# Performance work log

Hardware: AMD Instinct MI355X
Metric: run time of the kernel (lower is better)

## Reference

```python
import jax, jax.numpy as jnp
import numpy as np


def setup_inputs() -> dict:
    key = jax.random.key(0)
    k1, k2, k3 = jax.random.split(key, 3)
    B, M, K, C = 4, 64, 32, 256
    ch, red = K * K, 2
    x = jax.random.normal(k1, (B, M, K, C), dtype=jnp.float32)
    # 1x1 conv weights (bias=False): squeeze spatial dims -> plain matrices
    W1 = jax.random.normal(k2, (ch // red, ch), dtype=jnp.float32) * 0.02
    W2 = jax.random.normal(k3, (ch, ch // red), dtype=jnp.float32) * 0.02
    return {"x": x, "W1": W1, "W2": W2}


def reference(x, W1, W2):
    B, M, K, C = x.shape
    # ---- Pearson correlation (Bessel-corrected), matches self.pearson ----
    cen = x - x.mean(axis=-1, keepdims=True)                       # [B,M,K,C]
    cov = jnp.einsum('bmic,bmjc->bmij', cen, cen) / (C - 1)         # [B,M,K,K]
    std = jnp.sqrt(jnp.sum(cen * cen, axis=-1) / (C - 1))           # [B,M,K]
    adj = cov / (std[..., :, None] * std[..., None, :])             # [B,M,K,K]
    # ---- attention scores: concat([x_i, pos*x_j]) then avgpool over 2C ----
    # pos = 1 where x_i == x_j elementwise else 2
    xi = x[:, :, :, None, :]                                        # [B,M,K,1,C]
    xj = x[:, :, None, :, :]                                        # [B,M,1,K,C]
    pos = jnp.where(xi == xj, jnp.float32(1.0), jnp.float32(2.0))   # [B,M,K,K,C]
    # AdaptiveAvgPool2d((None,1)) over the 2C concat = mean of both halves
    pooled = 0.5 * (x.mean(-1)[:, :, :, None] + jnp.mean(pos * xj, axis=-1))  # [B,M,K,K]
    # conv input channel index is i*K+j -> reshape to [B, K*K, M]
    p = pooled.transpose(0, 2, 3, 1).reshape(B, K * K, M)
    h = jax.nn.gelu(jnp.einsum('oc,bcm->bom', W1, p), approximate=False)
    e = jax.nn.sigmoid(jnp.einsum('oc,bcm->bom', W2, h))            # [B,K*K,M]
    e = e.transpose(0, 2, 1).reshape(B, M, K, K)
    # ---- masked softmax + aggregation ----
    NEG = jnp.float32(-9e15)
    attention = jax.nn.softmax(jnp.where(adj > 0, e, NEG), axis=-1)
    out = jnp.einsum('bmij,bmjc->bmic', attention, x)               # [B,M,K,C]
    return out, adj
```

## Files before the change

kernel.cpp:

```cpp
#include <hip/hip_runtime.h>
#include <math.h>

#define KK 32
#define CC 256

__global__ __launch_bounds__(256) void prep_kernel(
    const float* __restrict__ x, float* __restrict__ mean_ws,
    float* __restrict__ adj_out)
{
    __shared__ float xs[KK][258];
    __shared__ float part8[256];
    __shared__ float meanv[KK];
    __shared__ float covm[KK][KK + 1];
    __shared__ float stdv[KK];

    const int t  = threadIdx.x;
    const int bm = blockIdx.x;
    const int b  = bm >> 6, m = bm & 63;
    const float* xp = x + (size_t)bm * (KK * CC);

    #pragma unroll
    for (int s = 0; s < 8; ++s) {
        const int e = s * 1024 + t * 4;
        const float4 v = *(const float4*)(xp + e);
        const int i = e >> 8, col = e & 255;
        xs[i][col] = v.x; xs[i][col + 1] = v.y;
        xs[i][col + 2] = v.z; xs[i][col + 3] = v.w;
    }
    __syncthreads();
    {
        const int i = t >> 3, part = t & 7;
        float s = 0.f;
        const int c0 = part * 32;
        #pragma unroll
        for (int c = 0; c < 32; ++c) s += xs[i][c0 + c];
        part8[t] = s;
    }
    __syncthreads();
    if (t < KK) {
        float s = 0.f;
        #pragma unroll
        for (int k = 0; k < 8; ++k) s += part8[t * 8 + k];
        meanv[t] = s * (1.0f / CC);
        mean_ws[(size_t)(b * 32 + t) * 64 + m] = meanv[t];
    }
    __syncthreads();
    {
        const int r = t >> 3, c0 = (t & 7) * 32;
        const float mv = meanv[r];
        #pragma unroll
        for (int c = 0; c < 32; ++c) xs[r][c0 + c] -= mv;
    }
    __syncthreads();
    if (t < 136) {
        int rem = t, r = 0;
        while (rem >= 16 - r) { rem -= 16 - r; ++r; }
        const int ti = r, tj = r + rem;
        const int i0 = 2 * ti, i1 = i0 + 1, j0 = 2 * tj, j1 = j0 + 1;
        float c00 = 0.f, c01 = 0.f, c10 = 0.f, c11 = 0.f;
        for (int c = 0; c < CC; c += 2) {
            const float2 a0 = *(const float2*)&xs[i0][c];
            const float2 a1 = *(const float2*)&xs[i1][c];
            const float2 b0 = *(const float2*)&xs[j0][c];
            const float2 b1 = *(const float2*)&xs[j1][c];
            c00 += a0.x * b0.x; c00 += a0.y * b0.y;
            c01 += a0.x * b1.x; c01 += a0.y * b1.y;
            c10 += a1.x * b0.x; c10 += a1.y * b0.y;
            c11 += a1.x * b1.x; c11 += a1.y * b1.y;
        }
        c00 *= (1.0f / (CC - 1)); c01 *= (1.0f / (CC - 1));
        c10 *= (1.0f / (CC - 1)); c11 *= (1.0f / (CC - 1));
        covm[i0][j0] = c00; covm[i0][j1] = c01;
        covm[i1][j0] = c10; covm[i1][j1] = c11;
        covm[j0][i0] = c00; covm[j1][i0] = c01;
        covm[j0][i1] = c10; covm[j1][i1] = c11;
    }
    __syncthreads();
    if (t < KK) stdv[t] = sqrtf(covm[t][t]);
    __syncthreads();
    #pragma unroll
    for (int k = 0; k < 4; ++k) {
        const int pair = t + k * 256;
        const int i = pair >> 5, j = pair & 31;
        adj_out[(size_t)bm * 1024 + pair] = covm[i][j] / (stdv[i] * stdv[j]);
    }
}

__global__ __launch_bounds__(64) void mlp1_kernel(
    const float* __restrict__ W1, const float* __restrict__ mean_ws,
    float* __restrict__ h_ws)
{
    __shared__ float rowlds[4][1056];
    __shared__ float Al[4][32];
    const int t  = threadIdx.x;
    const int b  = blockIdx.y;
    const int ob = blockIdx.x * 4;

    const float* wr = W1 + (size_t)ob * 1024;
    #pragma unroll
    for (int u = 0; u < 16; ++u) {
        const int e4 = t + u * 64;
        const int q  = e4 >> 8;
        const int e  = (e4 & 255) * 4;
        const float4 v = *(const float4*)(wr + q * 1024 + e);
        const int f = (e >> 5) * 33 + (e & 31);
        rowlds[q][f] = v.x; rowlds[q][f + 1] = v.y;
        rowlds[q][f + 2] = v.z; rowlds[q][f + 3] = v.w;
    }
    __syncthreads();
    {
        const int k = t & 31, qh = t >> 5;
        #pragma unroll
        for (int qq = 0; qq < 2; ++qq) {
            const int q = qh + qq * 2;
            float rs = 0.f, cs = 0.f;
            #pragma unroll
            for (int j = 0; j < 32; ++j) rs += rowlds[q][k * 33 + j];
            #pragma unroll
            for (int i = 0; i < 32; ++i) cs += rowlds[q][i * 33 + k];
            Al[q][k] = 0.5f * rs + cs - 0.5f * rowlds[q][k * 34];
        }
    }
    __syncthreads();
    const int m = t;
    float mr[32];
    #pragma unroll
    for (int k = 0; k < 32; ++k) mr[k] = mean_ws[(size_t)(b * 32 + k) * 64 + m];
    #pragma unroll
    for (int q = 0; q < 4; ++q) {
        float a = 0.f;
        #pragma unroll
        for (int k = 0; k < 32; ++k) a += Al[q][k] * mr[k];
        const float g = 0.5f * a * (1.0f + erff(a * 0.70710678118654752f));
        h_ws[(size_t)(b * 512 + ob + q) * 64 + m] = g;
    }
}

__global__ __launch_bounds__(256) void mlp2_kernel(
    const float* __restrict__ W2, const float* __restrict__ h_ws,
    float* __restrict__ e_ws)
{
    __shared__ float W2s[16][512];
    const int m  = threadIdx.x;
    const int ow = threadIdx.y;
    const int b  = blockIdx.y;
    const int ob = blockIdx.x * 16;

    {
        const int t = ow * 64 + m;
        const float* src = W2 + (size_t)ob * 512;
        #pragma unroll
        for (int u = 0; u < 8; ++u) {
            const int e4 = t + u * 256;
            const float4 v = *(const float4*)(src + e4 * 4);
            *(float4*)&W2s[e4 >> 7][(e4 & 127) * 4] = v;
        }
    }
    __syncthreads();

    const float* hb = h_ws + (size_t)b * 512 * 64 + m;
    float acc[4] = {0.f, 0.f, 0.f, 0.f};
    const int ol = ow * 4;

    for (int c = 0; c < 512; c += 4) {
        const float hv0 = hb[(size_t)(c + 0) * 64];
        const float hv1 = hb[(size_t)(c + 1) * 64];
        const float hv2 = hb[(size_t)(c + 2) * 64];
        const float hv3 = hb[(size_t)(c + 3) * 64];
        #pragma unroll
        for (int q = 0; q < 4; ++q) {
            const float4 w = *(const float4*)&W2s[ol + q][c];
            acc[q] += w.x * hv0;
            acc[q] += w.y * hv1;
            acc[q] += w.z * hv2;
            acc[q] += w.w * hv3;
        }
    }
    float4 sv;
    sv.x = 1.0f / (1.0f + expf(-acc[0]));
    sv.y = 1.0f / (1.0f + expf(-acc[1]));
    sv.z = 1.0f / (1.0f + expf(-acc[2]));
    sv.w = 1.0f / (1.0f + expf(-acc[3]));
    *(float4*)&e_ws[(size_t)(b * 64 + m) * 1024 + ob + ol] = sv;
}

__global__ __launch_bounds__(256) void softmax_out_kernel(
    const float* __restrict__ x, const float* __restrict__ e_ws,
    const float* __restrict__ adj, float* __restrict__ out)
{
    __shared__ float xs[KK][260];
    __shared__ float att[KK][KK + 1];
    const int bm = blockIdx.x;
    const int b  = bm >> 6, m = bm & 63;
    const int t  = threadIdx.x;
    const float* xp = x + (size_t)bm * (KK * CC);

    #pragma unroll
    for (int s = 0; s < 8; ++s) {
        const int e = s * 1024 + t * 4;
        const float4 v = *(const float4*)(xp + e);
        *(float4*)&xs[e >> 8][e & 255] = v;
    }
    {
        const int p0 = 4 * t;
        const float4 ev4 = *(const float4*)&e_ws[(size_t)(b * 64 + m) * 1024 + p0];
        const float4 aj4 = *(const float4*)&adj[(size_t)bm * 1024 + p0];
        const int i = p0 >> 5, j0 = p0 & 31;
        att[i][j0]     = (aj4.x > 0.f) ? ev4.x : -INFINITY;
        att[i][j0 + 1] = (aj4.y > 0.f) ? ev4.y : -INFINITY;
        att[i][j0 + 2] = (aj4.z > 0.f) ? ev4.z : -INFINITY;
        att[i][j0 + 3] = (aj4.w > 0.f) ? ev4.w : -INFINITY;
    }
    __syncthreads();
    if (t < KK) {
        float mx = -INFINITY;
        #pragma unroll
        for (int j = 0; j < KK; ++j) mx = fmaxf(mx, att[t][j]);
        float s = 0.f;
        #pragma unroll
        for (int j = 0; j < KK; ++j) {
            const float v = expf(att[t][j] - mx);
            att[t][j] = v;
            s += v;
        }
        const float inv = 1.0f / s;
        #pragma unroll
        for (int j = 0; j < KK; ++j) att[t][j] *= inv;
    }
    __syncthreads();

    const int c8 = t & 31, iq = t >> 5;
    const int i0 = iq * 4;
    const int cA = 4 * c8, cB = 128 + 4 * c8;
    float4 accA[4], accB[4];
    #pragma unroll
    for (int r = 0; r < 4; ++r) {
        accA[r] = make_float4(0.f, 0.f, 0.f, 0.f);
        accB[r] = make_float4(0.f, 0.f, 0.f, 0.f);
    }
    for (int j = 0; j < KK; ++j) {
        const float4 xa = *(const float4*)&xs[j][cA];
        const float4 xb = *(const float4*)&xs[j][cB];
        #pragma unroll
        for (int r = 0; r < 4; ++r) {
            const float av = att[i0 + r][j];
            accA[r].x += av * xa.x; accA[r].y += av * xa.y;
            accA[r].z += av * xa.z; accA[r].w += av * xa.w;
            accB[r].x += av * xb.x; accB[r].y += av * xb.y;
            accB[r].z += av * xb.z; accB[r].w += av * xb.w;
        }
    }
    float* op = out + (size_t)bm * (KK * CC);
    #pragma unroll
    for (int r = 0; r < 4; ++r) {
        *(float4*)(op + (size_t)(i0 + r) * CC + cA) = accA[r];
        *(float4*)(op + (size_t)(i0 + r) * CC + cB) = accB[r];
    }
}

extern "C" void kernel_launch(void* const* d_in, const int* in_sizes, int n_in,
                              void* d_out, int out_size, void* d_ws, size_t ws_size,
                              hipStream_t stream) {
    const float* x  = (const float*)d_in[0];
    const float* W1 = (const float*)d_in[1];
    const float* W2 = (const float*)d_in[2];
    float* out     = (float*)d_out;
    float* adj_out = out + (size_t)4 * 64 * 32 * 256;

    float* mean_ws = (float*)d_ws;
    float* h_ws    = mean_ws + 8192;
    float* e_ws    = h_ws + 131072;

    prep_kernel<<<256, 256, 0, stream>>>(x, mean_ws, adj_out);
    mlp1_kernel<<<dim3(128, 4), 64, 0, stream>>>(W1, mean_ws, h_ws);
    mlp2_kernel<<<dim3(64, 4), dim3(64, 4), 0, stream>>>(W2, h_ws, e_ws);
    softmax_out_kernel<<<256, 256, 0, stream>>>(x, e_ws, adj_out, out);
}
```

Measured before the change: 100.5 us.

## Fold W1 reduction into prep kernel and transpose h layout for vector loads

Extra blocks appended to the prep kernel now reduce W1 into a compact 512x32 matrix A once, reusing the shared memory through a union. Previously each mlp1 block recomputed this reduction for every batch. A new h_kernel computes GELU(A·mean) per (b,m) and writes h in [b,m,o] layout, so the e kernel can read contiguous float4 rows instead of strided scalars. A few unroll pragmas are also added. The cost is an extra workspace buffer and a changed dependency layout between kernels.

```diff
diff --git a/kernel.cpp b/kernel.cpp
--- a/kernel.cpp
+++ b/kernel.cpp
@@ -4,17 +4,52 @@
 #define KK 32
 #define CC 256
 
+union PrepSMem {
+    struct {
+        float xs[KK][258];
+        float covm[KK][KK + 1];
+        float part8[256];
+        float meanv[KK];
+        float stdv[KK];
+    } p;
+    float rowlds[8][1056];
+};
+
 __global__ __launch_bounds__(256) void prep_kernel(
-    const float* __restrict__ x, float* __restrict__ mean_ws,
+    const float* __restrict__ x, const float* __restrict__ W1,
+    float* __restrict__ mean_ws, float* __restrict__ A_ws,
     float* __restrict__ adj_out)
 {
-    __shared__ float xs[KK][258];
-    __shared__ float part8[256];
-    __shared__ float meanv[KK];
-    __shared__ float covm[KK][KK + 1];
-    __shared__ float stdv[KK];
-
-    const int t  = threadIdx.x;
+    __shared__ PrepSMem sm;
+    const int t = threadIdx.x;
+
+    if (blockIdx.x >= 256) {
+        const int ab = blockIdx.x - 256;
+        const float* wr = W1 + (size_t)ab * 8 * 1024;
+        #pragma unroll
+        for (int u = 0; u < 8; ++u) {
+            const int e4 = t + u * 256;
+            const int q  = e4 >> 8;
+            const int e  = (e4 & 255) * 4;
+            const float4 v = *(const float4*)(wr + q * 1024 + e);
+            const int f = (e >> 5) * 33 + (e & 31);
+            sm.rowlds[q][f] = v.x; sm.rowlds[q][f + 1] = v.y;
+            sm.rowlds[q][f + 2] = v.z; sm.rowlds[q][f + 3] = v.w;
+        }
+        __syncthreads();
+        {
+            const int k = t & 31, q = t >> 5;
+            float rs = 0.f, cs = 0.f;
+            #pragma unroll
+            for (int j = 0; j < 32; ++j) rs += sm.rowlds[q][k * 33 + j];
+            #pragma unroll
+            for (int i = 0; i < 32; ++i) cs += sm.rowlds[q][i * 33 + k];
+            A_ws[(size_t)(ab * 8 + q) * 32 + k] =
+                0.5f * rs + cs - 0.5f * sm.rowlds[q][k * 34];
+        }
+        return;
+    }
+
     const int bm = blockIdx.x;
     const int b  = bm >> 6, m = bm & 63;
     const float* xp = x + (size_t)bm * (KK * CC);
@@ -24,8 +59,8 @@
         const int e = s * 1024 + t * 4;
         const float4 v = *(const float4*)(xp + e);
         const int i = e >> 8, col = e & 255;
-        xs[i][col] = v.x; xs[i][col + 1] = v.y;
-        xs[i][col + 2] = v.z; xs[i][col + 3] = v.w;
+        sm.p.xs[i][col] = v.x; sm.p.xs[i][col + 1] = v.y;
+        sm.p.xs[i][col + 2] = v.z; sm.p.xs[i][col + 3] = v.w;
     }
     __syncthreads();
     {
@@ -33,23 +68,23 @@
         float s = 0.f;
         const int c0 = part * 32;
         #pragma unroll
-        for (int c = 0; c < 32; ++c) s += xs[i][c0 + c];
-        part8[t] = s;
+        for (int c = 0; c < 32; ++c) s += sm.p.xs[i][c0 + c];
+        sm.p.part8[t] = s;
     }
     __syncthreads();
     if (t < KK) {
         float s = 0.f;
         #pragma unroll
-        for (int k = 0; k < 8; ++k) s += part8[t * 8 + k];
-        meanv[t] = s * (1.0f / CC);
-        mean_ws[(size_t)(b * 32 + t) * 64 + m] = meanv[t];
+        for (int k = 0; k < 8; ++k) s += sm.p.part8[t * 8 + k];
+        sm.p.meanv[t] = s * (1.0f / CC);
+        mean_ws[(size_t)(b * 32 + t) * 64 + m] = sm.p.meanv[t];
     }
     __syncthreads();
     {
         const int r = t >> 3, c0 = (t & 7) * 32;
-        const float mv = meanv[r];
-        #pragma unroll
-        for (int c = 0; c < 32; ++c) xs[r][c0 + c] -= mv;
+        const float mv = sm.p.meanv[r];
+        #pragma unroll
+        for (int c = 0; c < 32; ++c) sm.p.xs[r][c0 + c] -= mv;
     }
     __syncthreads();
     if (t < 136) {
@@ -58,11 +93,12 @@
         const int ti = r, tj = r + rem;
         const int i0 = 2 * ti, i1 = i0 + 1, j0 = 2 * tj, j1 = j0 + 1;
         float c00 = 0.f, c01 = 0.f, c10 = 0.f, c11 = 0.f;
+        #pragma unroll 4
         for (int c = 0; c < CC; c += 2) {
-            const float2 a0 = *(const float2*)&xs[i0][c];
-            const float2 a1 = *(const float2*)&xs[i1][c];
-            const float2 b0 = *(const float2*)&xs[j0][c];
-            const float2 b1 = *(const float2*)&xs[j1][c];
+            const float2 a0 = *(const float2*)&sm.p.xs[i0][c];
+            const float2 a1 = *(const float2*)&sm.p.xs[i1][c];
+            const float2 b0 = *(const float2*)&sm.p.xs[j0][c];
+            const float2 b1 = *(const float2*)&sm.p.xs[j1][c];
             c00 += a0.x * b0.x; c00 += a0.y * b0.y;
             c01 += a0.x * b1.x; c01 += a0.y * b1.y;
             c10 += a1.x * b0.x; c10 += a1.y * b0.y;
@@ -70,73 +106,56 @@
         }
         c00 *= (1.0f / (CC - 1)); c01 *= (1.0f / (CC - 1));
         c10 *= (1.0f / (CC - 1)); c11 *= (1.0f / (CC - 1));
-        covm[i0][j0] = c00; covm[i0][j1] = c01;
-        covm[i1][j0] = c10; covm[i1][j1] = c11;
-        covm[j0][i0] = c00; covm[j1][i0] = c01;
-        covm[j0][i1] = c10; covm[j1][i1] = c11;
-    }
-    __syncthreads();
-    if (t < KK) stdv[t] = sqrtf(covm[t][t]);
+        sm.p.covm[i0][j0] = c00; sm.p.covm[i0][j1] = c01;
+        sm.p.covm[i1][j0] = c10; sm.p.covm[i1][j1] = c11;
+        sm.p.covm[j0][i0] = c00; sm.p.covm[j1][i0] = c01;
+        sm.p.covm[j0][i1] = c10; sm.p.covm[j1][i1] = c11;
+    }
+    __syncthreads();
+    if (t < KK) sm.p.stdv[t] = sqrtf(sm.p.covm[t][t]);
     __syncthreads();
     #pragma unroll
     for (int k = 0; k < 4; ++k) {
         const int pair = t + k * 256;
         const int i = pair >> 5, j = pair & 31;
-        adj_out[(size_t)bm * 1024 + pair] = covm[i][j] / (stdv[i] * stdv[j]);
-    }
-}
-
-__global__ __launch_bounds__(64) void mlp1_kernel(
-    const float* __restrict__ W1, const float* __restrict__ mean_ws,
+        adj_out[(size_t)bm * 1024 + pair] =
+            sm.p.covm[i][j] / (sm.p.stdv[i] * sm.p.stdv[j]);
+    }
+}
+
+__global__ __launch_bounds__(256) void h_kernel(
+    const float* __restrict__ A_ws, const float* __restrict__ mean_ws,
     float* __restrict__ h_ws)
 {
-    __shared__ float rowlds[4][1056];
-    __shared__ float Al[4][32];
+    __shared__ float meanv[KK];
     const int t  = threadIdx.x;
-    const int b  = blockIdx.y;
-    const int ob = blockIdx.x * 4;
-
-    const float* wr = W1 + (size_t)ob * 1024;
-    #pragma unroll
-    for (int u = 0; u < 16; ++u) {
-        const int e4 = t + u * 64;
-        const int q  = e4 >> 8;
-        const int e  = (e4 & 255) * 4;
-        const float4 v = *(const float4*)(wr + q * 1024 + e);
-        const int f = (e >> 5) * 33 + (e & 31);
-        rowlds[q][f] = v.x; rowlds[q][f + 1] = v.y;
-        rowlds[q][f + 2] = v.z; rowlds[q][f + 3] = v.w;
-    }
-    __syncthreads();
-    {
-        const int k = t & 31, qh = t >> 5;
-        #pragma unroll
-        for (int qq = 0; qq < 2; ++qq) {
-            const int q = qh + qq * 2;
-            float rs = 0.f, cs = 0.f;
-            #pragma unroll
-            for (int j = 0; j < 32; ++j) rs += rowlds[q][k * 33 + j];
-            #pragma unroll
-            for (int i = 0; i < 32; ++i) cs += rowlds[q][i * 33 + k];
-            Al[q][k] = 0.5f * rs + cs - 0.5f * rowlds[q][k * 34];
-        }
-    }
-    __syncthreads();
-    const int m = t;
-    float mr[32];
-    #pragma unroll
-    for (int k = 0; k < 32; ++k) mr[k] = mean_ws[(size_t)(b * 32 + k) * 64 + m];
-    #pragma unroll
-    for (int q = 0; q < 4; ++q) {
-        float a = 0.f;
-        #pragma unroll
-        for (int k = 0; k < 32; ++k) a += Al[q][k] * mr[k];
-        const float g = 0.5f * a * (1.0f + erff(a * 0.70710678118654752f));
-        h_ws[(size_t)(b * 512 + ob + q) * 64 + m] = g;
-    }
-}
-
-__global__ __launch_bounds__(256) void mlp2_kernel(
+    const int bm = blockIdx.x;
+    const int b  = bm >> 6, m = bm & 63;
+    if (t < KK) meanv[t] = mean_ws[(size_t)(b * 32 + t) * 64 + m];
+    __syncthreads();
+
+    const int o0 = t * 2;
+    const float* a0 = A_ws + (size_t)o0 * 32;
+    const float* a1 = a0 + 32;
+    float r0[32], r1[32];
+    #pragma unroll
+    for (int u = 0; u < 8; ++u) {
+        *(float4*)&r0[u * 4] = *(const float4*)(a0 + u * 4);
+        *(float4*)&r1[u * 4] = *(const float4*)(a1 + u * 4);
+    }
+    float s0 = 0.f, s1 = 0.f;
+    #pragma unroll
+    for (int k = 0; k < 32; ++k) {
+        s0 += r0[k] * meanv[k];
+        s1 += r1[k] * meanv[k];
+    }
+    const float g0 = 0.5f * s0 * (1.0f + erff(s0 * 0.70710678118654752f));
+    const float g1 = 0.5f * s1 * (1.0f + erff(s1 * 0.70710678118654752f));
+    float2 st; st.x = g0; st.y = g1;
+    *(float2*)&h_ws[(size_t)(b * 64 + m) * 512 + o0] = st;
+}
+
+__global__ __launch_bounds__(256) void e_kernel(
     const float* __restrict__ W2, const float* __restrict__ h_ws,
     float* __restrict__ e_ws)
 {
@@ -158,22 +177,20 @@
     }
     __syncthreads();
 
-    const float* hb = h_ws + (size_t)b * 512 * 64 + m;
+    const float* hb = h_ws + (size_t)(b * 64 + m) * 512;
     float acc[4] = {0.f, 0.f, 0.f, 0.f};
     const int ol = ow * 4;
 
+    #pragma unroll 4
     for (int c = 0; c < 512; c += 4) {
-        const float hv0 = hb[(size_t)(c + 0) * 64];
-        const float hv1 = hb[(size_t)(c + 1) * 64];
-        const float hv2 = hb[(size_t)(c + 2) * 64];
-        const float hv3 = hb[(size_t)(c + 3) * 64];
+        const float4 hv = *(const float4*)(hb + c);
         #pragma unroll
         for (int q = 0; q < 4; ++q) {
             const float4 w = *(const float4*)&W2s[ol + q][c];
-            acc[q] += w.x * hv0;
-            acc[q] += w.y * hv1;
-            acc[q] += w.z * hv2;
-            acc[q] += w.w * hv3;
+            acc[q] += w.x * hv.x;
+            acc[q] += w.y * hv.y;
+            acc[q] += w.z * hv.z;
+            acc[q] += w.w * hv.w;
         }
     }
     float4 sv;
@@ -238,6 +255,7 @@
         accA[r] = make_float4(0.f, 0.f, 0.f, 0.f);
         accB[r] = make_float4(0.f, 0.f, 0.f, 0.f);
     }
+    #pragma unroll 2
     for (int j = 0; j < KK; ++j) {
         const float4 xa = *(const float4*)&xs[j][cA];
         const float4 xb = *(const float4*)&xs[j][cB];
@@ -268,11 +286,12 @@
     float* adj_out = out + (size_t)4 * 64 * 32 * 256;
 
     float* mean_ws = (float*)d_ws;
-    float* h_ws    = mean_ws + 8192;
+    float* A_ws    = mean_ws + 8192;
+    float* h_ws    = A_ws + 16384;
     float* e_ws    = h_ws + 131072;
 
-    prep_kernel<<<256, 256, 0, stream>>>(x, mean_ws, adj_out);
-    mlp1_kernel<<<dim3(128, 4), 64, 0, stream>>>(W1, mean_ws, h_ws);
-    mlp2_kernel<<<dim3(64, 4), dim3(64, 4), 0, stream>>>(W2, h_ws, e_ws);
+    prep_kernel<<<320, 256, 0, stream>>>(x, W1, mean_ws, A_ws, adj_out);
+    h_kernel<<<256, 256, 0, stream>>>(A_ws, mean_ws, h_ws);
+    e_kernel<<<dim3(64, 4), dim3(64, 4), 0, stream>>>(W2, h_ws, e_ws);
     softmax_out_kernel<<<256, 256, 0, stream>>>(x, e_ws, adj_out, out);
 }
```

Measured after the change: 105.8 us. +5.3%, slower.

## Fuse all four stages into one cooperative kernel with grid syncs

Applied to the files above, without the earlier changes.

Replaces the four separate launches (prep, mlp1, mlp2, softmax/aggregate) with one cooperative kernel of 256 blocks that uses grid.sync() between phases. x stays resident in shared memory across phases, so it is not reloaded for the final aggregation. The adjacency is kept in LDS instead of being re-read from global memory. The W1 reduction is spread across blocks through a workspace, and each block computes its own h column from its local means. This removes launch gaps and redundant global traffic, in exchange for the cost of grid-wide barriers and a larger LDS footprint per block.

```diff
diff --git a/kernel.cpp b/kernel.cpp
--- a/kernel.cpp
+++ b/kernel.cpp
@@ -1,33 +1,69 @@
 #include <hip/hip_runtime.h>
+#include <hip/hip_cooperative_groups.h>
 #include <math.h>
 
 #define KK 32
 #define CC 256
 
-__global__ __launch_bounds__(256) void prep_kernel(
-    const float* __restrict__ x, float* __restrict__ mean_ws,
-    float* __restrict__ adj_out)
+namespace cg = cooperative_groups;
+
+union UPhase {
+    float rowlds[2][1056];
+    float A_ch[256][33];
+    float W2s[16][512];
+    float att[KK][KK + 1];
+};
+
+__global__ __launch_bounds__(256) void fused_kernel(
+    const float* __restrict__ x, const float* __restrict__ W1,
+    const float* __restrict__ W2, float* __restrict__ A_ws,
+    float* __restrict__ h_ws, float* __restrict__ e_ws,
+    float* __restrict__ out, float* __restrict__ adj_out)
 {
-    __shared__ float xs[KK][258];
+    __shared__ float xs[KK][260];
+    __shared__ float xc[KK][258];
+    __shared__ UPhase U;
+    __shared__ float covm[KK][KK + 1];
     __shared__ float part8[256];
     __shared__ float meanv[KK];
-    __shared__ float covm[KK][KK + 1];
     __shared__ float stdv[KK];
 
+    cg::grid_group grid = cg::this_grid();
     const int t  = threadIdx.x;
     const int bm = blockIdx.x;
     const int b  = bm >> 6, m = bm & 63;
+
+    {
+        const float* wr = W1 + (size_t)bm * 2048;
+        #pragma unroll
+        for (int u = 0; u < 2; ++u) {
+            const int e4 = t + u * 256;
+            const int q  = e4 >> 8;
+            const int e  = (e4 & 255) * 4;
+            const float4 v = *(const float4*)(wr + q * 1024 + e);
+            const int f = (e >> 5) * 33 + (e & 31);
+            U.rowlds[q][f] = v.x; U.rowlds[q][f + 1] = v.y;
+            U.rowlds[q][f + 2] = v.z; U.rowlds[q][f + 3] = v.w;
+        }
+    }
     const float* xp = x + (size_t)bm * (KK * CC);
-
     #pragma unroll
     for (int s = 0; s < 8; ++s) {
         const int e = s * 1024 + t * 4;
         const float4 v = *(const float4*)(xp + e);
-        const int i = e >> 8, col = e & 255;
-        xs[i][col] = v.x; xs[i][col + 1] = v.y;
-        xs[i][col + 2] = v.z; xs[i][col + 3] = v.w;
-    }
-    __syncthreads();
+        *(float4*)&xs[e >> 8][e & 255] = v;
+    }
+    __syncthreads();
+    if (t < 64) {
+        const int k = t & 31, q = t >> 5;
+        float rs = 0.f, cs = 0.f;
+        #pragma unroll
+        for (int j = 0; j < 32; ++j) rs += U.rowlds[q][k * 33 + j];
+        #pragma unroll
+        for (int i = 0; i < 32; ++i) cs += U.rowlds[q][i * 33 + k];
+        A_ws[(size_t)(bm * 2 + q) * 32 + k] =
+            0.5f * rs + cs - 0.5f * U.rowlds[q][k * 34];
+    }
     {
         const int i = t >> 3, part = t & 7;
         float s = 0.f;
@@ -42,14 +78,13 @@
         #pragma unroll
         for (int k = 0; k < 8; ++k) s += part8[t * 8 + k];
         meanv[t] = s * (1.0f / CC);
-        mean_ws[(size_t)(b * 32 + t) * 64 + m] = meanv[t];
     }
     __syncthreads();
     {
         const int r = t >> 3, c0 = (t & 7) * 32;
         const float mv = meanv[r];
         #pragma unroll
-        for (int c = 0; c < 32; ++c) xs[r][c0 + c] -= mv;
+        for (int c = 0; c < 32; ++c) xc[r][c0 + c] = xs[r][c0 + c] - mv;
     }
     __syncthreads();
     if (t < 136) {
@@ -58,11 +93,12 @@
         const int ti = r, tj = r + rem;
         const int i0 = 2 * ti, i1 = i0 + 1, j0 = 2 * tj, j1 = j0 + 1;
         float c00 = 0.f, c01 = 0.f, c10 = 0.f, c11 = 0.f;
+        #pragma unroll 4
         for (int c = 0; c < CC; c += 2) {
-            const float2 a0 = *(const float2*)&xs[i0][c];
-            const float2 a1 = *(const float2*)&xs[i1][c];
-            const float2 b0 = *(const float2*)&xs[j0][c];
-            const float2 b1 = *(const float2*)&xs[j1][c];
+            const float2 a0 = *(const float2*)&xc[i0][c];
+            const float2 a1 = *(const float2*)&xc[i1][c];
+            const float2 b0 = *(const float2*)&xc[j0][c];
+            const float2 b1 = *(const float2*)&xc[j1][c];
             c00 += a0.x * b0.x; c00 += a0.y * b0.y;
             c01 += a0.x * b1.x; c01 += a0.y * b1.y;
             c10 += a1.x * b0.x; c10 += a1.y * b0.y;
@@ -82,179 +118,125 @@
     for (int k = 0; k < 4; ++k) {
         const int pair = t + k * 256;
         const int i = pair >> 5, j = pair & 31;
-        adj_out[(size_t)bm * 1024 + pair] = covm[i][j] / (stdv[i] * stdv[j]);
-    }
-}
-
-__global__ __launch_bounds__(64) void mlp1_kernel(
-    const float* __restrict__ W1, const float* __restrict__ mean_ws,
-    float* __restrict__ h_ws)
-{
-    __shared__ float rowlds[4][1056];
-    __shared__ float Al[4][32];
-    const int t  = threadIdx.x;
-    const int b  = blockIdx.y;
-    const int ob = blockIdx.x * 4;
-
-    const float* wr = W1 + (size_t)ob * 1024;
-    #pragma unroll
-    for (int u = 0; u < 16; ++u) {
-        const int e4 = t + u * 64;
-        const int q  = e4 >> 8;
-        const int e  = (e4 & 255) * 4;
-        const float4 v = *(const float4*)(wr + q * 1024 + e);
-        const int f = (e >> 5) * 33 + (e & 31);
-        rowlds[q][f] = v.x; rowlds[q][f + 1] = v.y;
-        rowlds[q][f + 2] = v.z; rowlds[q][f + 3] = v.w;
-    }
-    __syncthreads();
-    {
-        const int k = t & 31, qh = t >> 5;
-        #pragma unroll
-        for (int qq = 0; qq < 2; ++qq) {
-            const int q = qh + qq * 2;
-            float rs = 0.f, cs = 0.f;
-            #pragma unroll
-            for (int j = 0; j < 32; ++j) rs += rowlds[q][k * 33 + j];
-            #pragma unroll
-            for (int i = 0; i < 32; ++i) cs += rowlds[q][i * 33 + k];
-            Al[q][k] = 0.5f * rs + cs - 0.5f * rowlds[q][k * 34];
-        }
-    }
-    __syncthreads();
-    const int m = t;
-    float mr[32];
-    #pragma unroll
-    for (int k = 0; k < 32; ++k) mr[k] = mean_ws[(size_t)(b * 32 + k) * 64 + m];
-    #pragma unroll
-    for (int q = 0; q < 4; ++q) {
-        float a = 0.f;
-        #pragma unroll
-        for (int k = 0; k < 32; ++k) a += Al[q][k] * mr[k];
-        const float g = 0.5f * a * (1.0f + erff(a * 0.70710678118654752f));
-        h_ws[(size_t)(b * 512 + ob + q) * 64 + m] = g;
-    }
-}
-
-__global__ __launch_bounds__(256) void mlp2_kernel(
-    const float* __restrict__ W2, const float* __restrict__ h_ws,
-    float* __restrict__ e_ws)
-{
-    __shared__ float W2s[16][512];
-    const int m  = threadIdx.x;
-    const int ow = threadIdx.y;
-    const int b  = blockIdx.y;
-    const int ob = blockIdx.x * 16;
-
-    {
-        const int t = ow * 64 + m;
+        const float av = covm[i][j] / (stdv[i] * stdv[j]);
+        adj_out[(size_t)bm * 1024 + pair] = av;
+        covm[i][j] = av;
+    }
+    grid.sync();
+
+    for (int ch = 0; ch < 2; ++ch) {
+        if (ch) __syncthreads();
+        const float* ap = A_ws + (size_t)ch * 8192;
+        #pragma unroll
+        for (int u = 0; u < 8; ++u) {
+            const int e4 = t + u * 256;
+            const float4 v = *(const float4*)(ap + e4 * 4);
+            const int ol = e4 >> 3, k0 = (e4 & 7) * 4;
+            U.A_ch[ol][k0]     = v.x; U.A_ch[ol][k0 + 1] = v.y;
+            U.A_ch[ol][k0 + 2] = v.z; U.A_ch[ol][k0 + 3] = v.w;
+        }
+        __syncthreads();
+        float s = 0.f;
+        #pragma unroll
+        for (int k = 0; k < 32; ++k) s += U.A_ch[t][k] * meanv[k];
+        const float g = 0.5f * s * (1.0f + erff(s * 0.70710678118654752f));
+        h_ws[(size_t)(b * 512 + ch * 256 + t) * 64 + m] = g;
+    }
+    grid.sync();
+
+    {
+        const int b3 = bm >> 6;
+        const int ob = (bm & 63) * 16;
+        const int m3 = t & 63, ow = t >> 6, ol = ow * 4;
         const float* src = W2 + (size_t)ob * 512;
         #pragma unroll
         for (int u = 0; u < 8; ++u) {
             const int e4 = t + u * 256;
             const float4 v = *(const float4*)(src + e4 * 4);
-            *(float4*)&W2s[e4 >> 7][(e4 & 127) * 4] = v;
-        }
-    }
-    __syncthreads();
-
-    const float* hb = h_ws + (size_t)b * 512 * 64 + m;
-    float acc[4] = {0.f, 0.f, 0.f, 0.f};
-    const int ol = ow * 4;
-
-    for (int c = 0; c < 512; c += 4) {
-        const float hv0 = hb[(size_t)(c + 0) * 64];
-        const float hv1 = hb[(size_t)(c + 1) * 64];
-        const float hv2 = hb[(size_t)(c + 2) * 64];
-        const float hv3 = hb[(size_t)(c + 3) * 64];
-        #pragma unroll
-        for (int q = 0; q < 4; ++q) {
-            const float4 w = *(const float4*)&W2s[ol + q][c];
-            acc[q] += w.x * hv0;
-            acc[q] += w.y * hv1;
-            acc[q] += w.z * hv2;
-            acc[q] += w.w * hv3;
-        }
-    }
-    float4 sv;
-    sv.x = 1.0f / (1.0f + expf(-acc[0]));
-    sv.y = 1.0f / (1.0f + expf(-acc[1]));
-    sv.z = 1.0f / (1.0f + expf(-acc[2]));
-    sv.w = 1.0f / (1.0f + expf(-acc[3]));
-    *(float4*)&e_ws[(size_t)(b * 64 + m) * 1024 + ob + ol] = sv;
-}
-
-__global__ __launch_bounds__(256) void softmax_out_kernel(
-    const float* __restrict__ x, const float* __restrict__ e_ws,
-    const float* __restrict__ adj, float* __restrict__ out)
-{
-    __shared__ float xs[KK][260];
-    __shared__ float att[KK][KK + 1];
-    const int bm = blockIdx.x;
-    const int b  = bm >> 6, m = bm & 63;
-    const int t  = threadIdx.x;
-    const float* xp = x + (size_t)bm * (KK * CC);
-
-    #pragma unroll
-    for (int s = 0; s < 8; ++s) {
-        const int e = s * 1024 + t * 4;
-        const float4 v = *(const float4*)(xp + e);
-        *(float4*)&xs[e >> 8][e & 255] = v;
-    }
+            *(float4*)&U.W2s[e4 >> 7][(e4 & 127) * 4] = v;
+        }
+        __syncthreads();
+        const float* hb = h_ws + (size_t)b3 * 512 * 64 + m3;
+        float acc[4] = {0.f, 0.f, 0.f, 0.f};
+        #pragma unroll 4
+        for (int c = 0; c < 512; c += 4) {
+            const float hv0 = hb[(size_t)(c + 0) * 64];
+            const float hv1 = hb[(size_t)(c + 1) * 64];
+            const float hv2 = hb[(size_t)(c + 2) * 64];
+            const float hv3 = hb[(size_t)(c + 3) * 64];
+            #pragma unroll
+            for (int q = 0; q < 4; ++q) {
+                const float4 w = *(const float4*)&U.W2s[ol + q][c];
+                acc[q] += w.x * hv0;
+                acc[q] += w.y * hv1;
+                acc[q] += w.z * hv2;
+                acc[q] += w.w * hv3;
+            }
+        }
+        float4 sv;
+        sv.x = 1.0f / (1.0f + expf(-acc[0]));
+        sv.y = 1.0f / (1.0f + expf(-acc[1]));
+        sv.z = 1.0f / (1.0f + expf(-acc[2]));
+        sv.w = 1.0f / (1.0f + expf(-acc[3]));
+        *(float4*)&e_ws[(size_t)(b3 * 64 + m3) * 1024 + ob + ol] = sv;
+    }
+    grid.sync();
+
     {
         const int p0 = 4 * t;
         const float4 ev4 = *(const float4*)&e_ws[(size_t)(b * 64 + m) * 1024 + p0];
-        const float4 aj4 = *(const float4*)&adj[(size_t)bm * 1024 + p0];
         const int i = p0 >> 5, j0 = p0 & 31;
-        att[i][j0]     = (aj4.x > 0.f) ? ev4.x : -INFINITY;
-        att[i][j0 + 1] = (aj4.y > 0.f) ? ev4.y : -INFINITY;
-        att[i][j0 + 2] = (aj4.z > 0.f) ? ev4.z : -INFINITY;
-        att[i][j0 + 3] = (aj4.w > 0.f) ? ev4.w : -INFINITY;
+        U.att[i][j0]     = (covm[i][j0]     > 0.f) ? ev4.x : -INFINITY;
+        U.att[i][j0 + 1] = (covm[i][j0 + 1] > 0.f) ? ev4.y : -INFINITY;
+        U.att[i][j0 + 2] = (covm[i][j0 + 2] > 0.f) ? ev4.z : -INFINITY;
+        U.att[i][j0 + 3] = (covm[i][j0 + 3] > 0.f) ? ev4.w : -INFINITY;
     }
     __syncthreads();
     if (t < KK) {
         float mx = -INFINITY;
         #pragma unroll
-        for (int j = 0; j < KK; ++j) mx = fmaxf(mx, att[t][j]);
+        for (int j = 0; j < KK; ++j) mx = fmaxf(mx, U.att[t][j]);
         float s = 0.f;
         #pragma unroll
         for (int j = 0; j < KK; ++j) {
-            const float v = expf(att[t][j] - mx);
-            att[t][j] = v;
+            const float v = expf(U.att[t][j] - mx);
+            U.att[t][j] = v;
             s += v;
         }
         const float inv = 1.0f / s;
         #pragma unroll
-        for (int j = 0; j < KK; ++j) att[t][j] *= inv;
-    }
-    __syncthreads();
-
-    const int c8 = t & 31, iq = t >> 5;
-    const int i0 = iq * 4;
-    const int cA = 4 * c8, cB = 128 + 4 * c8;
-    float4 accA[4], accB[4];
-    #pragma unroll
-    for (int r = 0; r < 4; ++r) {
-        accA[r] = make_float4(0.f, 0.f, 0.f, 0.f);
-        accB[r] = make_float4(0.f, 0.f, 0.f, 0.f);
-    }
-    for (int j = 0; j < KK; ++j) {
-        const float4 xa = *(const float4*)&xs[j][cA];
-        const float4 xb = *(const float4*)&xs[j][cB];
+        for (int j = 0; j < KK; ++j) U.att[t][j] *= inv;
+    }
+    __syncthreads();
+    {
+        const int c8 = t & 31, iq = t >> 5;
+        const int i0 = iq * 4;
+        const int cA = 4 * c8, cB = 128 + 4 * c8;
+        float4 accA[4], accB[4];
         #pragma unroll
         for (int r = 0; r < 4; ++r) {
-            const float av = att[i0 + r][j];
-            accA[r].x += av * xa.x; accA[r].y += av * xa.y;
-            accA[r].z += av * xa.z; accA[r].w += av * xa.w;
-            accB[r].x += av * xb.x; accB[r].y += av * xb.y;
-            accB[r].z += av * xb.z; accB[r].w += av * xb.w;
-        }
-    }
-    float* op = out + (size_t)bm * (KK * CC);
-    #pragma unroll
-    for (int r = 0; r < 4; ++r) {
-        *(float4*)(op + (size_t)(i0 + r) * CC + cA) = accA[r];
-        *(float4*)(op + (size_t)(i0 + r) * CC + cB) = accB[r];
+            accA[r] = make_float4(0.f, 0.f, 0.f, 0.f);
+            accB[r] = make_float4(0.f, 0.f, 0.f, 0.f);
+        }
+        #pragma unroll 2
+        for (int j = 0; j < KK; ++j) {
+            const float4 xa = *(const float4*)&xs[j][cA];
+            const float4 xb = *(const float4*)&xs[j][cB];
+            #pragma unroll
+            for (int r = 0; r < 4; ++r) {
+                const float av = U.att[i0 + r][j];
+                accA[r].x += av * xa.x; accA[r].y += av * xa.y;
+                accA[r].z += av * xa.z; accA[r].w += av * xa.w;
+                accB[r].x += av * xb.x; accB[r].y += av * xb.y;
+                accB[r].z += av * xb.z; accB[r].w += av * xb.w;
+            }
+        }
+        float* op = out + (size_t)bm * (KK * CC);
+        #pragma unroll
+        for (int r = 0; r < 4; ++r) {
+            *(float4*)(op + (size_t)(i0 + r) * CC + cA) = accA[r];
+            *(float4*)(op + (size_t)(i0 + r) * CC + cB) = accB[r];
+        }
     }
 }
 
@@ -267,12 +249,12 @@
     float* out     = (float*)d_out;
     float* adj_out = out + (size_t)4 * 64 * 32 * 256;
 
-    float* mean_ws = (float*)d_ws;
-    float* h_ws    = mean_ws + 8192;
-    float* e_ws    = h_ws + 131072;
-
-    prep_kernel<<<256, 256, 0, stream>>>(x, mean_ws, adj_out);
-    mlp1_kernel<<<dim3(128, 4), 64, 0, stream>>>(W1, mean_ws, h_ws);
-    mlp2_kernel<<<dim3(64, 4), dim3(64, 4), 0, stream>>>(W2, h_ws, e_ws);
-    softmax_out_kernel<<<256, 256, 0, stream>>>(x, e_ws, adj_out, out);
+    float* A_ws = (float*)d_ws;
+    float* h_ws = A_ws + 16384;
+    float* e_ws = h_ws + 131072;
+
+    void* args[] = { (void*)&x, (void*)&W1, (void*)&W2, (void*)&A_ws,
+                     (void*)&h_ws, (void*)&e_ws, (void*)&out, (void*)&adj_out };
+    hipLaunchCooperativeKernel((void*)fused_kernel, dim3(256), dim3(256),
+                               args, 0, stream);
 }
```

After: 191.5 us. 90.5% more time.

## Fold W1 row reduction into prep kernel and fuse both MLP layers

Applied to the files above, without the earlier changes.

Moves the reduction of W1 rows into A coefficients into the prep kernel, with each of its 256 blocks handling 2 of the 512 rows. The two MLP kernels are merged into one kernel that builds the GELU hidden chunk in shared memory and immediately multiplies it by W2. This removes one kernel launch and the global round-trip of the h workspace. In exchange, each he_kernel block recomputes its batch's full h (512x64) redundantly, and the 64 blocks per batch each repeat that work. A few unroll pragmas are also added.

```diff
diff --git a/kernel.cpp b/kernel.cpp
--- a/kernel.cpp
+++ b/kernel.cpp
@@ -5,10 +5,12 @@
 #define CC 256
 
 __global__ __launch_bounds__(256) void prep_kernel(
-    const float* __restrict__ x, float* __restrict__ mean_ws,
+    const float* __restrict__ x, const float* __restrict__ W1,
+    float* __restrict__ mean_ws, float* __restrict__ A_ws,
     float* __restrict__ adj_out)
 {
     __shared__ float xs[KK][258];
+    __shared__ float rowlds[2][1056];
     __shared__ float part8[256];
     __shared__ float meanv[KK];
     __shared__ float covm[KK][KK + 1];
@@ -19,6 +21,19 @@
     const int b  = bm >> 6, m = bm & 63;
     const float* xp = x + (size_t)bm * (KK * CC);
 
+    {
+        const float* wr = W1 + (size_t)bm * 2048;
+        #pragma unroll
+        for (int u = 0; u < 2; ++u) {
+            const int e4 = t + u * 256;
+            const int q  = e4 >> 8;
+            const int e  = (e4 & 255) * 4;
+            const float4 v = *(const float4*)(wr + q * 1024 + e);
+            const int f = (e >> 5) * 33 + (e & 31);
+            rowlds[q][f] = v.x; rowlds[q][f + 1] = v.y;
+            rowlds[q][f + 2] = v.z; rowlds[q][f + 3] = v.w;
+        }
+    }
     #pragma unroll
     for (int s = 0; s < 8; ++s) {
         const int e = s * 1024 + t * 4;
@@ -28,6 +43,16 @@
         xs[i][col + 2] = v.z; xs[i][col + 3] = v.w;
     }
     __syncthreads();
+    if (t < 64) {
+        const int k = t & 31, q = t >> 5;
+        float rs = 0.f, cs = 0.f;
+        #pragma unroll
+        for (int j = 0; j < 32; ++j) rs += rowlds[q][k * 33 + j];
+        #pragma unroll
+        for (int i = 0; i < 32; ++i) cs += rowlds[q][i * 33 + k];
+        A_ws[(size_t)(bm * 2 + q) * 32 + k] =
+            0.5f * rs + cs - 0.5f * rowlds[q][k * 34];
+    }
     {
         const int i = t >> 3, part = t & 7;
         float s = 0.f;
@@ -58,6 +83,7 @@
         const int ti = r, tj = r + rem;
         const int i0 = 2 * ti, i1 = i0 + 1, j0 = 2 * tj, j1 = j0 + 1;
         float c00 = 0.f, c01 = 0.f, c10 = 0.f, c11 = 0.f;
+        #pragma unroll 4
         for (int c = 0; c < CC; c += 2) {
             const float2 a0 = *(const float2*)&xs[i0][c];
             const float2 a1 = *(const float2*)&xs[i1][c];
@@ -86,68 +112,23 @@
     }
 }
 
-__global__ __launch_bounds__(64) void mlp1_kernel(
-    const float* __restrict__ W1, const float* __restrict__ mean_ws,
-    float* __restrict__ h_ws)
-{
-    __shared__ float rowlds[4][1056];
-    __shared__ float Al[4][32];
-    const int t  = threadIdx.x;
-    const int b  = blockIdx.y;
-    const int ob = blockIdx.x * 4;
-
-    const float* wr = W1 + (size_t)ob * 1024;
-    #pragma unroll
-    for (int u = 0; u < 16; ++u) {
-        const int e4 = t + u * 64;
-        const int q  = e4 >> 8;
-        const int e  = (e4 & 255) * 4;
-        const float4 v = *(const float4*)(wr + q * 1024 + e);
-        const int f = (e >> 5) * 33 + (e & 31);
-        rowlds[q][f] = v.x; rowlds[q][f + 1] = v.y;
-        rowlds[q][f + 2] = v.z; rowlds[q][f + 3] = v.w;
-    }
-    __syncthreads();
-    {
-        const int k = t & 31, qh = t >> 5;
-        #pragma unroll
-        for (int qq = 0; qq < 2; ++qq) {
-            const int q = qh + qq * 2;
-            float rs = 0.f, cs = 0.f;
-            #pragma unroll
-            for (int j = 0; j < 32; ++j) rs += rowlds[q][k * 33 + j];
-            #pragma unroll
-            for (int i = 0; i < 32; ++i) cs += rowlds[q][i * 33 + k];
-            Al[q][k] = 0.5f * rs + cs - 0.5f * rowlds[q][k * 34];
-        }
-    }
-    __syncthreads();
-    const int m = t;
-    float mr[32];
-    #pragma unroll
-    for (int k = 0; k < 32; ++k) mr[k] = mean_ws[(size_t)(b * 32 + k) * 64 + m];
-    #pragma unroll
-    for (int q = 0; q < 4; ++q) {
-        float a = 0.f;
-        #pragma unroll
-        for (int k = 0; k < 32; ++k) a += Al[q][k] * mr[k];
-        const float g = 0.5f * a * (1.0f + erff(a * 0.70710678118654752f));
-        h_ws[(size_t)(b * 512 + ob + q) * 64 + m] = g;
-    }
-}
-
-__global__ __launch_bounds__(256) void mlp2_kernel(
-    const float* __restrict__ W2, const float* __restrict__ h_ws,
-    float* __restrict__ e_ws)
+__global__ __launch_bounds__(256) void he_kernel(
+    const float* __restrict__ W2, const float* __restrict__ A_ws,
+    const float* __restrict__ mean_ws, float* __restrict__ e_ws)
 {
     __shared__ float W2s[16][512];
+    __shared__ float Ach[128][33];
+    __shared__ float hch[128][65];
+    __shared__ float mvs[32][65];
+
     const int m  = threadIdx.x;
     const int ow = threadIdx.y;
+    const int t  = ow * 64 + m;
     const int b  = blockIdx.y;
     const int ob = blockIdx.x * 16;
-
-    {
-        const int t = ow * 64 + m;
+    const int ol = ow * 4;
+
+    {
         const float* src = W2 + (size_t)ob * 512;
         #pragma unroll
         for (int u = 0; u < 8; ++u) {
@@ -156,26 +137,73 @@
             *(float4*)&W2s[e4 >> 7][(e4 & 127) * 4] = v;
         }
     }
-    __syncthreads();
-
-    const float* hb = h_ws + (size_t)b * 512 * 64 + m;
+    {
+        const float* src = mean_ws + (size_t)b * 2048;
+        #pragma unroll
+        for (int u = 0; u < 2; ++u) {
+            const int e4 = t + u * 256;
+            const float4 v = *(const float4*)(src + e4 * 4);
+            const int k = e4 >> 4, m0 = (e4 & 15) * 4;
+            mvs[k][m0] = v.x; mvs[k][m0 + 1] = v.y;
+            mvs[k][m0 + 2] = v.z; mvs[k][m0 + 3] = v.w;
+        }
+    }
+    __syncthreads();
+
+    float mr[32];
+    #pragma unroll
+    for (int k = 0; k < 32; ++k) mr[k] = mvs[k][m];
+
     float acc[4] = {0.f, 0.f, 0.f, 0.f};
-    const int ol = ow * 4;
-
-    for (int c = 0; c < 512; c += 4) {
-        const float hv0 = hb[(size_t)(c + 0) * 64];
-        const float hv1 = hb[(size_t)(c + 1) * 64];
-        const float hv2 = hb[(size_t)(c + 2) * 64];
-        const float hv3 = hb[(size_t)(c + 3) * 64];
-        #pragma unroll
-        for (int q = 0; q < 4; ++q) {
-            const float4 w = *(const float4*)&W2s[ol + q][c];
-            acc[q] += w.x * hv0;
-            acc[q] += w.y * hv1;
-            acc[q] += w.z * hv2;
-            acc[q] += w.w * hv3;
-        }
-    }
+
+    for (int cc = 0; cc < 4; ++cc) {
+        const int c0 = cc * 128;
+        {
+            const float* src = A_ws + (size_t)c0 * 32;
+            #pragma unroll
+            for (int u = 0; u < 4; ++u) {
+                const int e4 = t + u * 256;
+                const float4 v = *(const float4*)(src + e4 * 4);
+                const int row = e4 >> 3, k0 = (e4 & 7) * 4;
+                Ach[row][k0]     = v.x; Ach[row][k0 + 1] = v.y;
+                Ach[row][k0 + 2] = v.z; Ach[row][k0 + 3] = v.w;
+            }
+        }
+        __syncthreads();
+        {
+            #pragma unroll 4
+            for (int i = 0; i < 32; ++i) {
+                const int cl = ow * 32 + i;
+                float s = 0.f;
+                #pragma unroll
+                for (int k = 0; k < 32; ++k) s += Ach[cl][k] * mr[k];
+                const float g =
+                    0.5f * s * (1.0f + erff(s * 0.70710678118654752f));
+                hch[cl][m] = g;
+            }
+        }
+        __syncthreads();
+        {
+            #pragma unroll 4
+            for (int cl = 0; cl < 128; cl += 4) {
+                const int c = c0 + cl;
+                const float hv0 = hch[cl + 0][m];
+                const float hv1 = hch[cl + 1][m];
+                const float hv2 = hch[cl + 2][m];
+                const float hv3 = hch[cl + 3][m];
+                #pragma unroll
+                for (int q = 0; q < 4; ++q) {
+                    const float4 w = *(const float4*)&W2s[ol + q][c];
+                    acc[q] += w.x * hv0;
+                    acc[q] += w.y * hv1;
+                    acc[q] += w.z * hv2;
+                    acc[q] += w.w * hv3;
+                }
+            }
+        }
+        __syncthreads();
+    }
+
     float4 sv;
     sv.x = 1.0f / (1.0f + expf(-acc[0]));
     sv.y = 1.0f / (1.0f + expf(-acc[1]));
@@ -238,6 +266,7 @@
         accA[r] = make_float4(0.f, 0.f, 0.f, 0.f);
         accB[r] = make_float4(0.f, 0.f, 0.f, 0.f);
     }
+    #pragma unroll 2
     for (int j = 0; j < KK; ++j) {
         const float4 xa = *(const float4*)&xs[j][cA];
         const float4 xb = *(const float4*)&xs[j][cB];
@@ -268,11 +297,10 @@
     float* adj_out = out + (size_t)4 * 64 * 32 * 256;
 
     float* mean_ws = (float*)d_ws;
-    float* h_ws    = mean_ws + 8192;
-    float* e_ws    = h_ws + 131072;
-
-    prep_kernel<<<256, 256, 0, stream>>>(x, mean_ws, adj_out);
-    mlp1_kernel<<<dim3(128, 4), 64, 0, stream>>>(W1, mean_ws, h_ws);
-    mlp2_kernel<<<dim3(64, 4), dim3(64, 4), 0, stream>>>(W2, h_ws, e_ws);
+    float* A_ws    = mean_ws + 8192;
+    float* e_ws    = A_ws + 16384;
+
+    prep_kernel<<<256, 256, 0, stream>>>(x, W1, mean_ws, A_ws, adj_out);
+    he_kernel<<<dim3(64, 4), dim3(64, 4), 0, stream>>>(W2, A_ws, mean_ws, e_ws);
     softmax_out_kernel<<<256, 256, 0, stream>>>(x, e_ws, adj_out, out);
 }
```

Measured after the change: 144.0 us. 1.43x slower.
